# Kernel tuning notes

Hardware: AMD Instinct MI355X
Metric: run time of the kernel (lower is better)

## Reference

```python
import jax, jax.numpy as jnp
import numpy as np

B, C, Co, T, V, S, R, G = 64, 128, 128, 256, 25, 3, 16, 32
EPS = 1e-5


def setup_inputs() -> dict:
    key = jax.random.key(0)
    ks = jax.random.split(key, 12)
    sc = lambda fan: (2.0 / fan) ** 0.5  # kaiming fan_out-ish scale
    x = jax.random.normal(ks[0], (B, C, T, V), dtype=jnp.float32)
    Wq = jax.random.normal(ks[1], (S, R, C), dtype=jnp.float32) * sc(R)
    bq = jnp.zeros((S, R), dtype=jnp.float32)
    Wk = jax.random.normal(ks[2], (S, R, C), dtype=jnp.float32) * sc(R)
    bk = jnp.zeros((S, R), dtype=jnp.float32)
    Wv = jax.random.normal(ks[3], (S, Co, C), dtype=jnp.float32) * sc(Co)
    bv = jnp.zeros((S, Co), dtype=jnp.float32)
    Wr = jax.random.normal(ks[4], (S, Co, R), dtype=jnp.float32) * sc(Co)
    br = jnp.zeros((S, Co), dtype=jnp.float32)
    A = (jax.random.uniform(ks[5], (S, V, V), dtype=jnp.float32) < 0.15).astype(jnp.float32)
    alpha = jnp.zeros((1,), dtype=jnp.float32) + 0.1  # nonzero so relation path matters
    gn_w = jnp.full((Co,), 1e-6, dtype=jnp.float32)
    gn_b = jnp.zeros((Co,), dtype=jnp.float32)
    return {"x": x, "Wq": Wq, "bq": bq, "Wk": Wk, "bk": bk, "Wv": Wv, "bv": bv,
            "Wr": Wr, "br": br, "A": A, "alpha": alpha, "gn_w": gn_w, "gn_b": gn_b}


def reference(x, Wq, bq, Wk, bk, Wv, bv, Wr, br, A, alpha, gn_w, gn_b):
    # x: [B,C,T,V]. Mean over T commutes with the 1x1 conv (linear+bias).
    xm = x.mean(axis=2)                                          # [B,C,V]
    q = jnp.einsum('bcv,src->bsrv', xm, Wq) + bq[None, :, :, None]
    k = jnp.einsum('bcv,src->bsrv', xm, Wk) + bk[None, :, :, None]
    v = jnp.einsum('bctv,soc->bsotv', x, Wv) + bv[None, :, :, None, None]  # [B,S,Co,T,V]
    rel = jnp.tanh(q[..., :, None] - k[..., None, :])            # [B,S,R,V,V]
    relc = jnp.einsum('bsruv,sor->bsouv', rel, Wr) + br[None, :, :, None, None]
    relc = relc * alpha[0] + A[None, :, None, :, :]              # [B,S,Co,V,V]
    out = jnp.einsum('bsouv,bsotv->botu', relc, v)               # sum over subsets fused
    # GroupNorm(G, Co)
    o = out.reshape(B, G, Co // G, T, V)
    mu = o.mean(axis=(2, 3, 4), keepdims=True)
    var = ((o - mu) ** 2).mean(axis=(2, 3, 4), keepdims=True)
    o = ((o - mu) * jax.lax.rsqrt(var + EPS)).reshape(B, Co, T, V)
    o = o * gn_w[None, :, None, None] + gn_b[None, :, None, None]
    return jax.nn.relu(o + x)  # in==out -> identity residual
```

## Files before the change

kernel.cpp:

```cpp
#include <hip/hip_runtime.h>

#define BB 64
#define CC 128
#define CO 128
#define TTOT 256
#define VV 25
#define SS 3
#define RR 16
#define GG 32
#define EPSV 1e-5f
#define TT 8
#define NCOL 200
#define NCH 32

typedef __attribute__((ext_vector_type(8))) __bf16 bf16x8;
typedef __attribute__((ext_vector_type(4))) float f32x4;

static __device__ __forceinline__ ushort f2bf(float f) {
    unsigned u = __float_as_uint(f);
    u = (u + 0x7FFF + ((u >> 16) & 1)) >> 16;
    return (ushort)u;
}
static __device__ __forceinline__ float bf2f(ushort h) {
    return __uint_as_float(((unsigned)h) << 16);
}
static __device__ __forceinline__ f32x4 mfma16(bf16x8 a, bf16x8 b, f32x4 c) {
    return __builtin_amdgcn_mfma_f32_16x16x32_bf16(a, b, c, 0, 0, 0);
}

__global__ __launch_bounds__(256) void k_xmean(const float* __restrict__ x,
                                               float* __restrict__ xm) {
    int bc = blockIdx.x;
    const float* xp = x + (size_t)bc * (TTOT * VV);
    int t = threadIdx.x;
    float a[VV];
    const float* row = xp + t * VV;
#pragma unroll
    for (int v = 0; v < VV; ++v) a[v] = row[v];
#pragma unroll
    for (int v = 0; v < VV; ++v) {
#pragma unroll
        for (int off = 32; off > 0; off >>= 1) a[v] += __shfl_down(a[v], off, 64);
    }
    __shared__ float sm[4][VV];
    int wave = t >> 6, lane = t & 63;
    if (lane == 0) {
#pragma unroll
        for (int v = 0; v < VV; ++v) sm[wave][v] = a[v];
    }
    __syncthreads();
    if (t < VV) {
        float s = sm[0][t] + sm[1][t] + sm[2][t] + sm[3][t];
        xm[(size_t)bc * VV + t] = s * (1.0f / TTOT);
    }
}

__global__ __launch_bounds__(512) void k_pack_wv(const float* __restrict__ Wv,
                                                 ushort* __restrict__ wvp) {
    int t = blockIdx.x * 512 + threadIdx.x;
    int lane = t & 63;
    int ks = (t >> 6) & 3;
    int mt = (t >> 8) & 1;
    int ob = (t >> 9) & 3;
    int s  = t >> 11;
    int o  = ob * 32 + mt * 16 + (lane & 15);
    int c0 = (ks * 4 + (lane >> 4)) * 8;
    const float* src = Wv + ((size_t)s * CO + o) * CC + c0;
    float4 a = *(const float4*)src;
    float4 b = *(const float4*)(src + 4);
    union { ushort us[8]; int4 v; } u;
    u.us[0] = f2bf(a.x); u.us[1] = f2bf(a.y); u.us[2] = f2bf(a.z); u.us[3] = f2bf(a.w);
    u.us[4] = f2bf(b.x); u.us[5] = f2bf(b.y); u.us[6] = f2bf(b.z); u.us[7] = f2bf(b.w);
    *(int4*)&wvp[(size_t)t * 8] = u.v;
}

__global__ __launch_bounds__(512) void k_relc(const float* __restrict__ xm,
    const float* __restrict__ Wq, const float* __restrict__ bq,
    const float* __restrict__ Wk, const float* __restrict__ bk,
    const float* __restrict__ Wr, const float* __restrict__ br,
    const float* __restrict__ A, const float* __restrict__ alpha,
    ushort* __restrict__ rp) {
    int bs = blockIdx.x;
    int b = bs / SS, s = bs % SS;
    int tid = threadIdx.x;
    __shared__ float sxm[CC * VV];
    __shared__ float sq[RR * VV], sk[RR * VV];
    __shared__ float srel[RR][VV * VV];

    for (int i = tid; i < CC * VV; i += 512) sxm[i] = xm[(size_t)b * CC * VV + i];
    __syncthreads();

    if (tid < RR * VV) {
        int r = tid / VV, u = tid % VV;
        const float* wq = Wq + ((size_t)s * RR + r) * CC;
        const float* wk = Wk + ((size_t)s * RR + r) * CC;
        float aq = bq[s * RR + r], ak = bk[s * RR + r];
        for (int c = 0; c < CC; ++c) { float xv = sxm[c * VV + u]; aq += wq[c] * xv; ak += wk[c] * xv; }
        sq[tid] = aq; sk[tid] = ak;
    }
    __syncthreads();

    for (int i = tid; i < RR * VV * VV; i += 512) {
        int r = i / (VV * VV), uv = i % (VV * VV);
        srel[r][uv] = tanhf(sq[r * VV + uv / VV] - sk[r * VV + uv % VV]);
    }
    __syncthreads();

    float al = alpha[0];
    for (int i = tid; i < CO * VV; i += 512) {
        int o = i / VV, u = i % VV;
        float acc[VV];
        float base = br[s * CO + o];
#pragma unroll
        for (int k = 0; k < VV; ++k) acc[k] = base;
        const float* wr = Wr + ((size_t)s * CO + o) * RR;
#pragma unroll
        for (int r = 0; r < RR; ++r) {
            float w = wr[r];
            const float* sr = &srel[r][u * VV];
#pragma unroll
            for (int k = 0; k < VV; ++k) acc[k] += w * sr[k];
        }
        const float* Ab = A + (size_t)s * VV * VV + u * VV;
        ushort* dst = rp + (size_t)(bs * CO + o) * 1024 + (u >> 4) * 512 + (u & 15) * 8;
#pragma unroll
        for (int kb = 0; kb < 3; ++kb) {
            union { ushort us[8]; int4 v; } pk;
#pragma unroll
            for (int j = 0; j < 8; ++j) pk.us[j] = f2bf(acc[kb * 8 + j] * al + Ab[kb * 8 + j]);
            *(int4*)&dst[kb * 128] = pk.v;
        }
        dst[3 * 128] = f2bf(acc[24] * al + Ab[24]);
    }
}

__global__ __launch_bounds__(512, 4) void k_main(const float* __restrict__ x,
    const ushort* __restrict__ wvp, const float* __restrict__ bv,
    const ushort* __restrict__ rp, ushort* __restrict__ outw,
    float* __restrict__ stats) {
    int bid = blockIdx.x;
    int xcd = bid & 7, g = bid >> 3;
    int b = xcd + 8 * (g >> 5);
    int tch = g & 31;
    int tid = threadIdx.x;
    int wvi = tid >> 6;
    int lane = tid & 63;
    int g4 = lane >> 4;
    int l15 = lane & 15;

    __shared__ ushort s_xt[16 * 1600];
    __shared__ ushort s_v[32 * 256];
    __shared__ float s_bv[SS * CO];
    __shared__ float s_gstat[GG * 2];

    if (tid < GG * 2) s_gstat[tid] = 0.f;
    if (tid < SS * CO) s_bv[tid] = bv[tid];
    if (tid < 256) {
        int o = tid >> 3, t = tid & 7;
        *(int4*)&s_v[o * 256 + 3 * 64 + t * 8] = int4{0, 0, 0, 0};
    }

    const float* xb = x + ((size_t)b * CC) * (TTOT * VV) + tch * NCOL;
    for (int id = wvi; id < 64; id += 8) {
        int c8 = id >> 2, seg = id & 3;
        int n = seg * 64 + lane;
        if (n < NCOL) {
            float vals[8];
#pragma unroll
            for (int cc = 0; cc < 8; ++cc)
                vals[cc] = xb[(size_t)(c8 * 8 + cc) * (TTOT * VV) + n];
            union { ushort us[8]; int4 v4; } u;
#pragma unroll
            for (int cc = 0; cc < 8; ++cc) u.us[cc] = f2bf(vals[cc]);
            *(int4*)&s_xt[c8 * 1600 + n * 8] = u.v4;
        }
    }

    int mt = wvi & 1;
    int ntbase = wvi >> 1;

    for (int ob = 0; ob < 4; ++ob) {
        f32x4 acc2[4][2];
#pragma unroll
        for (int oi = 0; oi < 4; ++oi)
#pragma unroll
            for (int ut = 0; ut < 2; ++ut) acc2[oi][ut] = f32x4{0.f, 0.f, 0.f, 0.f};

        for (int s = 0; s < SS; ++s) {
            bf16x8 bfrag[4][2];
            const ushort* rb = rp + ((size_t)((b * SS + s) * CO) + ob * 32 + wvi * 4) * 1024
                             + g4 * 128 + l15 * 8;
#pragma unroll
            for (int oi = 0; oi < 4; ++oi) {
#pragma unroll
                for (int ut = 0; ut < 2; ++ut)
                    bfrag[oi][ut] = *(const bf16x8*)&rb[oi * 1024 + ut * 512];
            }
            bf16x8 afrag[4];
            const ushort* wb = wvp + ((size_t)((s * 4 + ob) * 2 + mt) * 4) * 512 + lane * 8;
#pragma unroll
            for (int ks = 0; ks < 4; ++ks)
                afrag[ks] = *(const bf16x8*)&wb[ks * 512];

            float bvr[4];
#pragma unroll
            for (int r = 0; r < 4; ++r)
                bvr[r] = s_bv[s * CO + ob * 32 + mt * 16 + g4 * 4 + r];

            __syncthreads();

            for (int nt = ntbase; nt < 13; nt += 4) {
                f32x4 d = f32x4{0.f, 0.f, 0.f, 0.f};
#pragma unroll
                for (int ks = 0; ks < 4; ++ks) {
                    bf16x8 bf = *(const bf16x8*)&s_xt[(ks * 4 + g4) * 1600 + (nt * 16 + l15) * 8];
                    d = mfma16(afrag[ks], bf, d);
                }
                int n = nt * 16 + l15;
                if (n < NCOL) {
                    int t = n / VV, k = n % VV;
                    int vb = (k >> 3) * 64 + t * 8 + (k & 7);
#pragma unroll
                    for (int r = 0; r < 4; ++r)
                        s_v[(mt * 16 + g4 * 4 + r) * 256 + vb] = f2bf(d[r] + bvr[r]);
                }
            }
            __syncthreads();

#pragma unroll
            for (int oi = 0; oi < 4; ++oi) {
                int ol = wvi * 4 + oi;
                bf16x8 av = *(const bf16x8*)&s_v[ol * 256 + g4 * 64 + (l15 & 7) * 8];
                acc2[oi][0] = mfma16(av, bfrag[oi][0], acc2[oi][0]);
                acc2[oi][1] = mfma16(av, bfrag[oi][1], acc2[oi][1]);
            }
        }

#pragma unroll
        for (int oi = 0; oi < 4; ++oi) {
            int o = ob * 32 + wvi * 4 + oi;
            float ps = 0.f, pq = 0.f;
            if (g4 < 2) {
#pragma unroll
                for (int ut = 0; ut < 2; ++ut) {
                    int u = ut * 16 + l15;
                    if (u < VV) {
#pragma unroll
                        for (int r = 0; r < 4; ++r) {
                            float val = acc2[oi][ut][r];
                            int t = g4 * 4 + r;
                            outw[(((size_t)b * CO + o) * TTOT + tch * TT + t) * VV + u] = f2bf(val);
                            ps += val; pq += val * val;
                        }
                    }
                }
            }
#pragma unroll
            for (int off = 32; off > 0; off >>= 1) {
                ps += __shfl_down(ps, off, 64);
                pq += __shfl_down(pq, off, 64);
            }
            if (lane == 0) {
                atomicAdd(&s_gstat[(o >> 2) * 2], ps);
                atomicAdd(&s_gstat[(o >> 2) * 2 + 1], pq);
            }
        }
    }
    __syncthreads();
    if (tid < GG * 2) atomicAdd(&stats[b * (GG * 2) + tid], s_gstat[tid]);
}

__global__ __launch_bounds__(256) void k_final(float* __restrict__ out,
    const ushort* __restrict__ outw, const float* __restrict__ x,
    const float* __restrict__ stats,
    const float* __restrict__ gw, const float* __restrict__ gb) {
    size_t i = ((size_t)blockIdx.x * 256 + threadIdx.x) * 4;
    int o = (int)((i / (TTOT * VV)) % CO);
    int b = (int)(i / ((size_t)CO * TTOT * VV));
    int gg = o >> 2;
    float s0 = stats[b * (GG * 2) + gg * 2];
    float s1 = stats[b * (GG * 2) + gg * 2 + 1];
    const float inv = 1.0f / (4 * TTOT * VV);
    float mu = s0 * inv;
    float var = s1 * inv - mu * mu;
    float rs = rsqrtf(var + EPSV) * gw[o];
    float sh = gb[o] - mu * rs;

    ushort4 rw = *(const ushort4*)(outw + i);
    float4 xr = *(const float4*)(x + i);
    float4 res;
    res.x = fmaxf(bf2f(rw.x) * rs + sh + xr.x, 0.f);
    res.y = fmaxf(bf2f(rw.y) * rs + sh + xr.y, 0.f);
    res.z = fmaxf(bf2f(rw.z) * rs + sh + xr.z, 0.f);
    res.w = fmaxf(bf2f(rw.w) * rs + sh + xr.w, 0.f);
    *(float4*)(out + i) = res;
}

extern "C" void kernel_launch(void* const* d_in, const int* in_sizes, int n_in,
                              void* d_out, int out_size, void* d_ws, size_t ws_size,
                              hipStream_t stream) {
    const float* x     = (const float*)d_in[0];
    const float* Wq    = (const float*)d_in[1];
    const float* bq    = (const float*)d_in[2];
    const float* Wk    = (const float*)d_in[3];
    const float* bk    = (const float*)d_in[4];
    const float* Wv    = (const float*)d_in[5];
    const float* bv    = (const float*)d_in[6];
    const float* Wr    = (const float*)d_in[7];
    const float* br    = (const float*)d_in[8];
    const float* A     = (const float*)d_in[9];
    const float* alpha = (const float*)d_in[10];
    const float* gw    = (const float*)d_in[11];
    const float* gb    = (const float*)d_in[12];
    float* out = (float*)d_out;

    float*  xm    = (float*)d_ws;
    float*  stats = xm + (size_t)BB * CC * VV;
    ushort* wvp   = (ushort*)(stats + (size_t)BB * GG * 2);
    ushort* rp    = wvp + 49152;
    ushort* outw  = rp + (size_t)BB * SS * CO * 1024;

    hipMemsetAsync(stats, 0, (size_t)BB * GG * 2 * sizeof(float), stream);
    hipMemsetAsync(rp, 0, (size_t)BB * SS * CO * 1024 * 2, stream);
    k_xmean<<<BB * CC, 256, 0, stream>>>(x, xm);
    k_pack_wv<<<12, 512, 0, stream>>>(Wv, wvp);
    k_relc<<<BB * SS, 512, 0, stream>>>(xm, Wq, bq, Wk, bk, Wr, br, A, alpha, rp);
    k_main<<<2048, 512, 0, stream>>>(x, wvp, bv, rp, outw, stats);
    k_final<<<(BB * CO * TTOT * VV) / (256 * 4), 256, 0, stream>>>(out, outw, x, stats, gw, gb);
}
```

Before: 408.0 us.

## Double-buffer V tile in main kernel and split relation kernel for parallelism

The main kernel now keeps a double-buffered LDS tile for the V projection. It computes the next stage's Wv×x MFMAs while consuming the current stage, so there is one barrier per stage instead of two. The relation kernel is split into a q/k kernel and a relcpack kernel launched over 8x more blocks, and that kernel writes the zero padding itself, which removes the large memset of rp. The V tile row is also compacted from 256 to 224 entries. In exchange there is an extra launch, an intermediate q/k buffer that aliases outw, and more register pressure from holding two A-fragment sets.

```diff
diff --git a/kernel.cpp b/kernel.cpp
--- a/kernel.cpp
+++ b/kernel.cpp
@@ -9,9 +9,6 @@
 #define RR 16
 #define GG 32
 #define EPSV 1e-5f
-#define TT 8
-#define NCOL 200
-#define NCH 32
 
 typedef __attribute__((ext_vector_type(8))) __bf16 bf16x8;
 typedef __attribute__((ext_vector_type(4))) float f32x4;
@@ -74,63 +71,78 @@
     *(int4*)&wvp[(size_t)t * 8] = u.v;
 }
 
-__global__ __launch_bounds__(512) void k_relc(const float* __restrict__ xm,
+__global__ __launch_bounds__(512) void k_qk(const float* __restrict__ xm,
     const float* __restrict__ Wq, const float* __restrict__ bq,
     const float* __restrict__ Wk, const float* __restrict__ bk,
-    const float* __restrict__ Wr, const float* __restrict__ br,
-    const float* __restrict__ A, const float* __restrict__ alpha,
-    ushort* __restrict__ rp) {
+    float* __restrict__ qb, float* __restrict__ kbuf) {
     int bs = blockIdx.x;
     int b = bs / SS, s = bs % SS;
     int tid = threadIdx.x;
     __shared__ float sxm[CC * VV];
-    __shared__ float sq[RR * VV], sk[RR * VV];
-    __shared__ float srel[RR][VV * VV];
-
     for (int i = tid; i < CC * VV; i += 512) sxm[i] = xm[(size_t)b * CC * VV + i];
     __syncthreads();
-
     if (tid < RR * VV) {
         int r = tid / VV, u = tid % VV;
         const float* wq = Wq + ((size_t)s * RR + r) * CC;
         const float* wk = Wk + ((size_t)s * RR + r) * CC;
         float aq = bq[s * RR + r], ak = bk[s * RR + r];
         for (int c = 0; c < CC; ++c) { float xv = sxm[c * VV + u]; aq += wq[c] * xv; ak += wk[c] * xv; }
-        sq[tid] = aq; sk[tid] = ak;
-    }
-    __syncthreads();
-
-    for (int i = tid; i < RR * VV * VV; i += 512) {
+        qb[bs * 400 + tid] = aq;
+        kbuf[bs * 400 + tid] = ak;
+    }
+}
+
+__global__ __launch_bounds__(256) void k_relcpack(const float* __restrict__ qb,
+    const float* __restrict__ kbuf, const float* __restrict__ Wr,
+    const float* __restrict__ br, const float* __restrict__ A,
+    const float* __restrict__ alpha, ushort* __restrict__ rp) {
+    int blk = blockIdx.x;
+    int oc = blk & 7, bs = blk >> 3;
+    int s = bs % SS;
+    int tid = threadIdx.x;
+    __shared__ float sq[RR * VV], sk[RR * VV];
+    __shared__ float srel[RR][VV * VV];
+    for (int i = tid; i < RR * VV; i += 256) { sq[i] = qb[bs * 400 + i]; sk[i] = kbuf[bs * 400 + i]; }
+    __syncthreads();
+    for (int i = tid; i < RR * VV * VV; i += 256) {
         int r = i / (VV * VV), uv = i % (VV * VV);
         srel[r][uv] = tanhf(sq[r * VV + uv / VV] - sk[r * VV + uv % VV]);
     }
     __syncthreads();
-
     float al = alpha[0];
-    for (int i = tid; i < CO * VV; i += 512) {
-        int o = i / VV, u = i % VV;
-        float acc[VV];
-        float base = br[s * CO + o];
-#pragma unroll
-        for (int k = 0; k < VV; ++k) acc[k] = base;
-        const float* wr = Wr + ((size_t)s * CO + o) * RR;
-#pragma unroll
-        for (int r = 0; r < RR; ++r) {
-            float w = wr[r];
-            const float* sr = &srel[r][u * VV];
-#pragma unroll
-            for (int k = 0; k < VV; ++k) acc[k] += w * sr[k];
-        }
-        const float* Ab = A + (size_t)s * VV * VV + u * VV;
-        ushort* dst = rp + (size_t)(bs * CO + o) * 1024 + (u >> 4) * 512 + (u & 15) * 8;
-#pragma unroll
-        for (int kb = 0; kb < 3; ++kb) {
-            union { ushort us[8]; int4 v; } pk;
-#pragma unroll
-            for (int j = 0; j < 8; ++j) pk.us[j] = f2bf(acc[kb * 8 + j] * al + Ab[kb * 8 + j]);
-            *(int4*)&dst[kb * 128] = pk.v;
-        }
-        dst[3 * 128] = f2bf(acc[24] * al + Ab[24]);
+    for (int i = tid; i < 512; i += 256) {
+        int ol = i >> 5, u = i & 31;
+        int o = oc * 16 + ol;
+        ushort* dst = rp + ((size_t)bs * CO + o) * 1024 + (u >> 4) * 512 + (u & 15) * 8;
+        if (u < VV) {
+            float acc[VV];
+            float base = br[s * CO + o];
+#pragma unroll
+            for (int k = 0; k < VV; ++k) acc[k] = base;
+            const float* wr = Wr + ((size_t)s * CO + o) * RR;
+#pragma unroll
+            for (int r = 0; r < RR; ++r) {
+                float w = wr[r];
+                const float* sr = &srel[r][u * VV];
+#pragma unroll
+                for (int k = 0; k < VV; ++k) acc[k] += w * sr[k];
+            }
+            const float* Ab = A + (size_t)s * VV * VV + u * VV;
+#pragma unroll
+            for (int kb4 = 0; kb4 < 4; ++kb4) {
+                union { ushort us[8]; int4 v; } pk;
+#pragma unroll
+                for (int j = 0; j < 8; ++j) {
+                    int kk = kb4 * 8 + j;
+                    pk.us[j] = (kk < VV) ? f2bf(acc[kk] * al + Ab[kk]) : (ushort)0;
+                }
+                *(int4*)&dst[kb4 * 128] = pk.v;
+            }
+        } else {
+#pragma unroll
+            for (int kb4 = 0; kb4 < 4; ++kb4)
+                *(int4*)&dst[kb4 * 128] = int4{0, 0, 0, 0};
+        }
     }
 }
 
@@ -149,22 +161,22 @@
     int l15 = lane & 15;
 
     __shared__ ushort s_xt[16 * 1600];
-    __shared__ ushort s_v[32 * 256];
+    __shared__ ushort s_v[2 * 32 * 224];
     __shared__ float s_bv[SS * CO];
     __shared__ float s_gstat[GG * 2];
 
     if (tid < GG * 2) s_gstat[tid] = 0.f;
     if (tid < SS * CO) s_bv[tid] = bv[tid];
     if (tid < 256) {
-        int o = tid >> 3, t = tid & 7;
-        *(int4*)&s_v[o * 256 + 3 * 64 + t * 8] = int4{0, 0, 0, 0};
-    }
-
-    const float* xb = x + ((size_t)b * CC) * (TTOT * VV) + tch * NCOL;
+        int pr = tid >> 2;
+        *(int4*)&s_v[pr * 224 + 192 + (tid & 3) * 8] = int4{0, 0, 0, 0};
+    }
+
+    const float* xb = x + ((size_t)b * CC) * (TTOT * VV) + tch * 200;
     for (int id = wvi; id < 64; id += 8) {
         int c8 = id >> 2, seg = id & 3;
         int n = seg * 64 + lane;
-        if (n < NCOL) {
+        if (n < 200) {
             float vals[8];
 #pragma unroll
             for (int cc = 0; cc < 8; ++cc)
@@ -176,66 +188,103 @@
         }
     }
 
-    int mt = wvi & 1;
-    int ntbase = wvi >> 1;
-
-    for (int ob = 0; ob < 4; ++ob) {
-        f32x4 acc2[4][2];
-#pragma unroll
-        for (int oi = 0; oi < 4; ++oi)
-#pragma unroll
-            for (int ut = 0; ut < 2; ++ut) acc2[oi][ut] = f32x4{0.f, 0.f, 0.f, 0.f};
-
-        for (int s = 0; s < SS; ++s) {
-            bf16x8 bfrag[4][2];
-            const ushort* rb = rp + ((size_t)((b * SS + s) * CO) + ob * 32 + wvi * 4) * 1024
-                             + g4 * 128 + l15 * 8;
-#pragma unroll
-            for (int oi = 0; oi < 4; ++oi) {
-#pragma unroll
-                for (int ut = 0; ut < 2; ++ut)
-                    bfrag[oi][ut] = *(const bf16x8*)&rb[oi * 1024 + ut * 512];
-            }
-            bf16x8 afrag[4];
-            const ushort* wb = wvp + ((size_t)((s * 4 + ob) * 2 + mt) * 4) * 512 + lane * 8;
-#pragma unroll
-            for (int ks = 0; ks < 4; ++ks)
-                afrag[ks] = *(const bf16x8*)&wb[ks * 512];
-
-            float bvr[4];
+    int n0 = wvi * 16 + l15;
+    int n1 = (wvi + 8) * 16 + l15;
+    bool v0 = (n0 < 200), v1 = (n1 < 200);
+    bool haveS1 = (wvi + 8) < 13;
+    int t0 = n0 / 25, k0 = n0 % 25;
+    int t1 = n1 / 25, k1 = n1 % 25;
+    int vb0 = (k0 < 24) ? ((k0 >> 3) * 64 + t0 * 8 + (k0 & 7)) : (192 + t0 * 4);
+    int vb1 = (k1 < 24) ? ((k1 >> 3) * 64 + t1 * 8 + (k1 & 7)) : (192 + t1 * 4);
+    int xo0 = (v0 ? n0 : 199) * 8;
+    int xo1 = (v1 ? n1 : 199) * 8;
+
+    __syncthreads();
+
+    f32x4 acc2[4][2];
+#pragma unroll
+    for (int oi = 0; oi < 4; ++oi) { acc2[oi][0] = f32x4{0,0,0,0}; acc2[oi][1] = f32x4{0,0,0,0}; }
+
+    bf16x8 afA[2][4], bfB[4][2];
+
+    auto load_af = [&](int st) {
+        int ss = st % 3, ob = st / 3;
+        const ushort* w0 = wvp + (size_t)((ss * 4 + ob) * 2) * 2048 + lane * 8;
+#pragma unroll
+        for (int ks = 0; ks < 4; ++ks) {
+            afA[0][ks] = *(const bf16x8*)&w0[ks * 512];
+            afA[1][ks] = *(const bf16x8*)&w0[2048 + ks * 512];
+        }
+    };
+    auto load_bf = [&](int st) {
+        int ss = st % 3, ob = st / 3;
+        const ushort* rb = rp + ((size_t)(b * SS + ss) * CO + ob * 32 + wvi * 4) * 1024
+                         + g4 * 128 + l15 * 8;
+#pragma unroll
+        for (int oi = 0; oi < 4; ++oi) {
+            bfB[oi][0] = *(const bf16x8*)&rb[oi * 1024];
+            bfB[oi][1] = *(const bf16x8*)&rb[oi * 1024 + 512];
+        }
+    };
+    auto do_g1 = [&](int st, ushort* vbuf) {
+        int ss = st % 3, ob = st / 3;
+        float bvv[2][4];
+#pragma unroll
+        for (int mt = 0; mt < 2; ++mt)
 #pragma unroll
             for (int r = 0; r < 4; ++r)
-                bvr[r] = s_bv[s * CO + ob * 32 + mt * 16 + g4 * 4 + r];
-
-            __syncthreads();
-
-            for (int nt = ntbase; nt < 13; nt += 4) {
-                f32x4 d = f32x4{0.f, 0.f, 0.f, 0.f};
-#pragma unroll
-                for (int ks = 0; ks < 4; ++ks) {
-                    bf16x8 bf = *(const bf16x8*)&s_xt[(ks * 4 + g4) * 1600 + (nt * 16 + l15) * 8];
-                    d = mfma16(afrag[ks], bf, d);
+                bvv[mt][r] = s_bv[ss * CO + ob * 32 + mt * 16 + g4 * 4 + r];
+        {
+            f32x4 d0 = f32x4{0,0,0,0}, d1 = f32x4{0,0,0,0};
+#pragma unroll
+            for (int ks = 0; ks < 4; ++ks) {
+                bf16x8 bx = *(const bf16x8*)&s_xt[(ks * 4 + g4) * 1600 + xo0];
+                d0 = mfma16(afA[0][ks], bx, d0);
+                d1 = mfma16(afA[1][ks], bx, d1);
+            }
+            if (v0) {
+#pragma unroll
+                for (int r = 0; r < 4; ++r) {
+                    vbuf[(g4 * 4 + r) * 224 + vb0]      = f2bf(d0[r] + bvv[0][r]);
+                    vbuf[(16 + g4 * 4 + r) * 224 + vb0] = f2bf(d1[r] + bvv[1][r]);
                 }
-                int n = nt * 16 + l15;
-                if (n < NCOL) {
-                    int t = n / VV, k = n % VV;
-                    int vb = (k >> 3) * 64 + t * 8 + (k & 7);
-#pragma unroll
-                    for (int r = 0; r < 4; ++r)
-                        s_v[(mt * 16 + g4 * 4 + r) * 256 + vb] = f2bf(d[r] + bvr[r]);
+            }
+        }
+        if (haveS1) {
+            f32x4 d0 = f32x4{0,0,0,0}, d1 = f32x4{0,0,0,0};
+#pragma unroll
+            for (int ks = 0; ks < 4; ++ks) {
+                bf16x8 bx = *(const bf16x8*)&s_xt[(ks * 4 + g4) * 1600 + xo1];
+                d0 = mfma16(afA[0][ks], bx, d0);
+                d1 = mfma16(afA[1][ks], bx, d1);
+            }
+            if (v1) {
+#pragma unroll
+                for (int r = 0; r < 4; ++r) {
+                    vbuf[(g4 * 4 + r) * 224 + vb1]      = f2bf(d0[r] + bvv[0][r]);
+                    vbuf[(16 + g4 * 4 + r) * 224 + vb1] = f2bf(d1[r] + bvv[1][r]);
                 }
             }
-            __syncthreads();
-
-#pragma unroll
-            for (int oi = 0; oi < 4; ++oi) {
-                int ol = wvi * 4 + oi;
-                bf16x8 av = *(const bf16x8*)&s_v[ol * 256 + g4 * 64 + (l15 & 7) * 8];
-                acc2[oi][0] = mfma16(av, bfrag[oi][0], acc2[oi][0]);
-                acc2[oi][1] = mfma16(av, bfrag[oi][1], acc2[oi][1]);
-            }
-        }
-
+        }
+    };
+    auto do_g2 = [&](const ushort* vbuf) {
+#pragma unroll
+        for (int oi = 0; oi < 4; ++oi) {
+            int ol = wvi * 4 + oi;
+            bf16x8 av;
+            if (g4 < 3) {
+                av = *(const bf16x8*)&vbuf[ol * 224 + g4 * 64 + (l15 & 7) * 8];
+            } else {
+                union { ushort us[8]; bf16x8 v; } u;
+                *(ushort4*)&u.us[0] = *(const ushort4*)&vbuf[ol * 224 + 192 + (l15 & 7) * 4];
+                u.us[4] = 0; u.us[5] = 0; u.us[6] = 0; u.us[7] = 0;
+                av = u.v;
+            }
+            acc2[oi][0] = mfma16(av, bfB[oi][0], acc2[oi][0]);
+            acc2[oi][1] = mfma16(av, bfB[oi][1], acc2[oi][1]);
+        }
+    };
+    auto do_epi = [&](int ob) {
 #pragma unroll
         for (int oi = 0; oi < 4; ++oi) {
             int o = ob * 32 + wvi * 4 + oi;
@@ -249,7 +298,7 @@
                         for (int r = 0; r < 4; ++r) {
                             float val = acc2[oi][ut][r];
                             int t = g4 * 4 + r;
-                            outw[(((size_t)b * CO + o) * TTOT + tch * TT + t) * VV + u] = f2bf(val);
+                            outw[(((size_t)b * CO + o) * TTOT + tch * 8 + t) * VV + u] = f2bf(val);
                             ps += val; pq += val * val;
                         }
                     }
@@ -264,7 +313,24 @@
                 atomicAdd(&s_gstat[(o >> 2) * 2], ps);
                 atomicAdd(&s_gstat[(o >> 2) * 2 + 1], pq);
             }
-        }
+            acc2[oi][0] = f32x4{0,0,0,0};
+            acc2[oi][1] = f32x4{0,0,0,0};
+        }
+    };
+
+    load_af(0);
+    do_g1(0, s_v);
+    for (int st = 0; st < 12; ++st) {
+        ushort* rbuf = s_v + (st & 1) * (32 * 224);
+        ushort* wbuf = s_v + ((st & 1) ^ 1) * (32 * 224);
+        __syncthreads();
+        load_bf(st);
+        if (st < 11) {
+            load_af(st + 1);
+            do_g1(st + 1, wbuf);
+        }
+        do_g2(rbuf);
+        if (st % 3 == 2) do_epi(st / 3);
     }
     __syncthreads();
     if (tid < GG * 2) atomicAdd(&stats[b * (GG * 2) + tid], s_gstat[tid]);
@@ -319,12 +385,14 @@
     ushort* wvp   = (ushort*)(stats + (size_t)BB * GG * 2);
     ushort* rp    = wvp + 49152;
     ushort* outw  = rp + (size_t)BB * SS * CO * 1024;
+    float*  qb    = (float*)outw;
+    float*  kbuf  = qb + (size_t)BB * SS * RR * VV;
 
     hipMemsetAsync(stats, 0, (size_t)BB * GG * 2 * sizeof(float), stream);
-    hipMemsetAsync(rp, 0, (size_t)BB * SS * CO * 1024 * 2, stream);
     k_xmean<<<BB * CC, 256, 0, stream>>>(x, xm);
     k_pack_wv<<<12, 512, 0, stream>>>(Wv, wvp);
-    k_relc<<<BB * SS, 512, 0, stream>>>(xm, Wq, bq, Wk, bk, Wr, br, A, alpha, rp);
+    k_qk<<<BB * SS, 512, 0, stream>>>(xm, Wq, bq, Wk, bk, qb, kbuf);
+    k_relcpack<<<BB * SS * 8, 256, 0, stream>>>(qb, kbuf, Wr, br, A, alpha, rp);
     k_main<<<2048, 512, 0, stream>>>(x, wvp, bv, rp, outw, stats);
     k_final<<<(BB * CO * TTOT * VV) / (256 * 4), 256, 0, stream>>>(out, outw, x, stats, gw, gb);
 }
```

Result: slower. 530.7 us (+30.1%).
